# Optimization experiments

Hardware: AMD Instinct MI355X
Metric: run time of the kernel (lower is better)

## Reference

```python
import jax, jax.numpy as jnp
import numpy as np

HEADS = 12
EMBED = 768
HEAD_DIM = EMBED // HEADS


def setup_inputs() -> dict:
    key = jax.random.key(0)
    kx, kw, kb = jax.random.split(key, 3)
    x = jax.random.normal(kx, (8, 1024, EMBED), dtype=jnp.float32)
    # nn.Linear(embed, 3*embed): weight (3E, E), bias (3E,)
    W_qkv = jax.random.normal(kw, (3 * EMBED, EMBED), dtype=jnp.float32) * (1.0 / np.sqrt(EMBED))
    b_qkv = jax.random.normal(kb, (3 * EMBED,), dtype=jnp.float32) * 0.01
    return {"x": x, "W_qkv": W_qkv, "b_qkv": b_qkv}


def reference(x, W_qkv, b_qkv):
    b, n, e = x.shape
    qkv = x @ W_qkv.T + b_qkv                       # (b, n, 3E)
    qkv = qkv.reshape(b, n, HEADS, 3 * HEAD_DIM)    # (b, n, h, 3d)
    q, k, v = jnp.split(qkv, 3, axis=-1)            # each (b, n, h, d)
    scores = jnp.einsum('bihd,bjhd->bijh', q, k) / np.sqrt(HEAD_DIM)
    attn = jax.nn.softmax(scores, axis=-2)          # softmax over keys j (dim=-2)
    out = jnp.einsum('bijh,bjhd->bihd', attn, v)
    return out.reshape(b, n, e)
```

## Files before the change

kernel.cpp:

```cpp
#include <hip/hip_runtime.h>
#include <hip/hip_bf16.h>
#include <cstdint>

#define BATCH 8
#define SEQ   1024
#define EMB   768
#define HEADS 12
#define HDIM  64
#define C3    2304
#define MROWS (BATCH*SEQ)
#define KSLC  (EMB / 16)
#define XPACK_BLOCKS (MROWS * KSLC / 256)
#define WPACK_BLOCKS (C3 * KSLC / 256)

typedef __attribute__((ext_vector_type(8)))  short bf16x8;
typedef __attribute__((ext_vector_type(4)))  short bf16x4;
typedef __attribute__((ext_vector_type(4)))  float f32x4;
typedef __attribute__((ext_vector_type(16))) float f32x16;

static __device__ inline short f2bf(float f) {
    union { float f; uint32_t u; } v; v.f = f;
    uint32_t u = v.u + 0x7fff + ((v.u >> 16) & 1);
    return (short)(u >> 16);
}

__global__ __launch_bounds__(256) void pack_bf16(const float* __restrict__ x,
                                                 short* __restrict__ xb2,
                                                 const float* __restrict__ W,
                                                 short* __restrict__ Wb2) {
    const float* in;
    short* out;
    int tid;
    if (blockIdx.x < XPACK_BLOCKS) {
        in = x; out = xb2;
        tid = blockIdx.x * 256 + threadIdx.x;
    } else {
        in = W; out = Wb2;
        tid = (blockIdx.x - XPACK_BLOCKS) * 256 + threadIdx.x;
    }
    const int r    = tid & 31;
    const int ks   = (tid >> 5) % KSLC;
    const int tile = tid / (KSLC * 32);
    const int row  = tile * 32 + r;

    const float* src = in + (size_t)row * EMB + ks * 16;
    float4 v0 = ((const float4*)src)[0];
    float4 v1 = ((const float4*)src)[1];
    float4 v2 = ((const float4*)src)[2];
    float4 v3 = ((const float4*)src)[3];
    bf16x8 o0 = { f2bf(v0.x), f2bf(v0.y), f2bf(v0.z), f2bf(v0.w),
                  f2bf(v1.x), f2bf(v1.y), f2bf(v1.z), f2bf(v1.w) };
    bf16x8 o1 = { f2bf(v2.x), f2bf(v2.y), f2bf(v2.z), f2bf(v2.w),
                  f2bf(v3.x), f2bf(v3.y), f2bf(v3.z), f2bf(v3.w) };
    short* dst = out + (size_t)tid * 16;
    *(bf16x8*)(dst)     = o0;
    *(bf16x8*)(dst + 8) = o1;
}

__global__ __launch_bounds__(256) void qkv_gemm_mfma(const short* __restrict__ xb2,
                                                     const short* __restrict__ Wb2,
                                                     const float* __restrict__ bias,
                                                     short* __restrict__ qkvb) {
    const int g    = blockIdx.x;
    const int xcd  = g & 7;
    const int ring = g >> 3;
    const int by   = xcd * 8 + (ring & 7);
    const int bx   = ring >> 3;

    const int t = threadIdx.x;
    const int w = t >> 6;
    const int lane = t & 63;
    const int l5  = lane >> 5;
    const int r31 = lane & 31;
    const int m0 = by * 128, n0 = bx * 128;
    const int wm = (w & 1) * 64, wn = (w >> 1) * 64;

    const int laneoff = r31 * 16 + l5 * 8;
    const short* pa0 = xb2 + ((size_t)((m0 + wm) >> 5) * KSLC) * 512 + laneoff;
    const short* pa1 = pa0 + (size_t)KSLC * 512;
    const short* pb0 = Wb2 + ((size_t)((n0 + wn) >> 5) * KSLC) * 512 + laneoff;
    const short* pb1 = pb0 + (size_t)KSLC * 512;

    f32x16 acc[2][2] = {};

    #pragma unroll 4
    for (int ks = 0; ks < KSLC; ++ks) {
        bf16x8 a0 = *(const bf16x8*)(pa0 + ks * 512);
        bf16x8 a1 = *(const bf16x8*)(pa1 + ks * 512);
        bf16x8 b0 = *(const bf16x8*)(pb0 + ks * 512);
        bf16x8 b1 = *(const bf16x8*)(pb1 + ks * 512);
        acc[0][0] = __builtin_amdgcn_mfma_f32_32x32x16_bf16(a0, b0, acc[0][0], 0, 0, 0);
        acc[0][1] = __builtin_amdgcn_mfma_f32_32x32x16_bf16(a0, b1, acc[0][1], 0, 0, 0);
        acc[1][0] = __builtin_amdgcn_mfma_f32_32x32x16_bf16(a1, b0, acc[1][0], 0, 0, 0);
        acc[1][1] = __builtin_amdgcn_mfma_f32_32x32x16_bf16(a1, b1, acc[1][1], 0, 0, 0);
    }

    float bsv[2], scl[2];
    #pragma unroll
    for (int nt = 0; nt < 2; ++nt) {
        int n = n0 + wn + nt * 32 + r31;
        bsv[nt] = bias[n];
        scl[nt] = ((n % 192) < 64) ? 0.125f : 1.0f;
    }
    #pragma unroll
    for (int mt = 0; mt < 2; ++mt)
        #pragma unroll
        for (int nt = 0; nt < 2; ++nt) {
            int n = n0 + wn + nt * 32 + r31;
            #pragma unroll
            for (int reg = 0; reg < 16; ++reg) {
                int row = (reg & 3) + 8 * (reg >> 2) + 4 * l5;
                int m = m0 + wm + mt * 32 + row;
                float v = (acc[mt][nt][reg] + bsv[nt]) * scl[nt];
                qkvb[(size_t)m * C3 + n] = f2bf(v);
            }
        }
}

__global__ __launch_bounds__(256) void v_transpose(const short* __restrict__ qkvb,
                                                   short* __restrict__ vt) {
    __shared__ int Lt[64][65];

    const int bh = blockIdx.x;
    const int jt = blockIdx.y;
    const int b = bh / HEADS, h = bh % HEADS;
    const int t = threadIdx.x;
    const int j0 = jt * 64;
    const size_t base = (size_t)b * SEQ * C3 + (size_t)h * 192 + 128;

    #pragma unroll
    for (int p = 0; p < 2; ++p) {
        int idx = p * 256 + t;
        int j = idx >> 3, d0 = (idx & 7) * 8;
        bf16x8 v = *(const bf16x8*)(qkvb + base + (size_t)(j0 + j) * C3 + d0);
        #pragma unroll
        for (int u = 0; u < 8; ++u)
            Lt[d0 + u][j] = (int)(unsigned short)v[u];
    }
    __syncthreads();
    #pragma unroll
    for (int p = 0; p < 2; ++p) {
        int idx = p * 256 + t;
        int d = idx >> 3, c8 = (idx & 7) * 8;
        bf16x8 o;
        #pragma unroll
        for (int u = 0; u < 8; ++u)
            o[u] = (short)Lt[d][c8 + u];
        *(bf16x8*)(vt + ((size_t)bh * 64 + d) * SEQ + j0 + c8) = o;
    }
}

#define LDP 72

__global__ __launch_bounds__(256, 3) void attn_mfma(const short* __restrict__ qkvb,
                                                    const short* __restrict__ vt,
                                                    float* __restrict__ out) {
    __shared__ short Ks[64][LDP];
    __shared__ short Vt[64][LDP];
    __shared__ short Ps[128][LDP];

    const int g    = blockIdx.x;
    const int qt   = g / (BATCH * HEADS);
    const int bh   = g % (BATCH * HEADS);
    const int b    = bh / HEADS;
    const int h    = bh % HEADS;
    const int t    = threadIdx.x;
    const int w    = t >> 6;
    const int lane = t & 63;
    const int c    = lane & 15;
    const int q    = lane >> 4;
    const int i0   = qt * 128;

    const size_t base = (size_t)b * SEQ * C3 + (size_t)h * 192;
    const short* vtb = vt + (size_t)bh * 64 * SEQ;

    #pragma unroll
    for (int p = 0; p < 4; ++p) {
        int idx = p * 256 + t;
        int i = idx >> 3, d0 = (idx & 7) << 3;
        *(bf16x8*)&Ps[i][d0] =
            *(const bf16x8*)(qkvb + base + (size_t)(i0 + i) * C3 + d0);
    }
    __syncthreads();
    bf16x8 aq[2][2];
    #pragma unroll
    for (int s = 0; s < 2; ++s) {
        aq[s][0] = *(bf16x8*)&Ps[w * 32 + s * 16 + c][q * 8];
        aq[s][1] = *(bf16x8*)&Ps[w * 32 + s * 16 + c][32 + q * 8];
    }

    f32x4 o[2][4] = {};
    float l_acc[2] = {0.f, 0.f};

    for (int kt = 0; kt < 16; ++kt) {
        const int j0 = kt * 64;
        __syncthreads();
        #pragma unroll
        for (int p = 0; p < 2; ++p) {
            int idx = p * 256 + t;
            int j = idx >> 3, d0 = (idx & 7) << 3;
            *(bf16x8*)&Ks[j][d0] =
                *(const bf16x8*)(qkvb + base + 64 + (size_t)(j0 + j) * C3 + d0);
        }
        #pragma unroll
        for (int p = 0; p < 2; ++p) {
            int idx = p * 256 + t;
            int d = idx >> 3, j8 = (idx & 7) << 3;
            *(bf16x8*)&Vt[d][j8] =
                *(const bf16x8*)(vtb + (size_t)d * SEQ + j0 + j8);
        }
        __syncthreads();

        bf16x8 ka[4][2];
        #pragma unroll
        for (int mt = 0; mt < 4; ++mt) {
            ka[mt][0] = *(bf16x8*)&Ks[mt * 16 + c][q * 8];
            ka[mt][1] = *(bf16x8*)&Ks[mt * 16 + c][32 + q * 8];
        }

        f32x4 s[2][4];
        #pragma unroll
        for (int ss = 0; ss < 2; ++ss)
            #pragma unroll
            for (int mt = 0; mt < 4; ++mt) {
                f32x4 acc = {0.f, 0.f, 0.f, 0.f};
                acc = __builtin_amdgcn_mfma_f32_16x16x32_bf16(ka[mt][0], aq[ss][0], acc, 0, 0, 0);
                acc = __builtin_amdgcn_mfma_f32_16x16x32_bf16(ka[mt][1], aq[ss][1], acc, 0, 0, 0);
                s[ss][mt] = acc;
            }

        #pragma unroll
        for (int ss = 0; ss < 2; ++ss)
            #pragma unroll
            for (int mt = 0; mt < 4; ++mt) {
                float p0 = __expf(s[ss][mt][0]);
                float p1 = __expf(s[ss][mt][1]);
                float p2 = __expf(s[ss][mt][2]);
                float p3 = __expf(s[ss][mt][3]);
                l_acc[ss] += (p0 + p1) + (p2 + p3);
                bf16x4 pw = { f2bf(p0), f2bf(p1), f2bf(p2), f2bf(p3) };
                *(bf16x4*)&Ps[w * 32 + ss * 16 + c][mt * 16 + 4 * q] = pw;
            }

        bf16x8 vb[4][2];
        #pragma unroll
        for (int dt = 0; dt < 4; ++dt) {
            vb[dt][0] = *(bf16x8*)&Vt[dt * 16 + c][q * 8];
            vb[dt][1] = *(bf16x8*)&Vt[dt * 16 + c][32 + q * 8];
        }

        #pragma unroll
        for (int ss = 0; ss < 2; ++ss) {
            bf16x8 ap0 = *(bf16x8*)&Ps[w * 32 + ss * 16 + c][q * 8];
            bf16x8 ap1 = *(bf16x8*)&Ps[w * 32 + ss * 16 + c][32 + q * 8];
            #pragma unroll
            for (int dt = 0; dt < 4; ++dt) {
                o[ss][dt] = __builtin_amdgcn_mfma_f32_16x16x32_bf16(ap0, vb[dt][0], o[ss][dt], 0, 0, 0);
                o[ss][dt] = __builtin_amdgcn_mfma_f32_16x16x32_bf16(ap1, vb[dt][1], o[ss][dt], 0, 0, 0);
            }
        }
    }

    float linv[2][4];
    #pragma unroll
    for (int ss = 0; ss < 2; ++ss) {
        float v = l_acc[ss];
        v += __shfl_xor(v, 16, 64);
        v += __shfl_xor(v, 32, 64);
        #pragma unroll
        for (int r = 0; r < 4; ++r)
            linv[ss][r] = 1.0f / __shfl(v, 4 * q + r, 64);
    }

    #pragma unroll
    for (int ss = 0; ss < 2; ++ss)
        #pragma unroll
        for (int dt = 0; dt < 4; ++dt)
            #pragma unroll
            for (int r = 0; r < 4; ++r) {
                int i = w * 32 + ss * 16 + q * 4 + r;
                out[((size_t)b * SEQ + i0 + i) * EMB + h * HDIM + dt * 16 + c]
                    = o[ss][dt][r] * linv[ss][r];
            }
}

extern "C" void kernel_launch(void* const* d_in, const int* in_sizes, int n_in,
                              void* d_out, int out_size, void* d_ws, size_t ws_size,
                              hipStream_t stream) {
    const float* x    = (const float*)d_in[0];
    const float* W    = (const float*)d_in[1];
    const float* bias = (const float*)d_in[2];
    float* out = (float*)d_out;

    short* xb2  = (short*)d_ws;
    short* Wb2  = xb2 + (size_t)MROWS * EMB;
    short* qkvb = Wb2 + (size_t)C3 * EMB;
    short* vt   = qkvb + (size_t)MROWS * C3;

    pack_bf16<<<XPACK_BLOCKS + WPACK_BLOCKS, 256, 0, stream>>>(x, xb2, W, Wb2);

    qkv_gemm_mfma<<<1152, 256, 0, stream>>>(xb2, Wb2, bias, qkvb);

    dim3 g2(BATCH * HEADS, SEQ / 64);
    v_transpose<<<g2, 256, 0, stream>>>(qkvb, vt);

    attn_mfma<<<BATCH * HEADS * (SEQ / 128), 256, 0, stream>>>(qkvb, vt, out);
}
```

Measured before the change: 169.3 us.

## Stage QKV GEMM tiles through double-buffered LDS with direct global-to-LDS loads

The QKV projection GEMM previously streamed each wave's operand fragments straight from global memory, so a fragment shared by waves was fetched once per wave. It now double-buffers 128x32 A and B tiles in shared memory using global_load_lds, so loads overlap compute and the four waves reuse one copy. The pack kernel now emits a tile-contiguous, XOR-swizzled layout so the LDS reads avoid bank conflicts, and the MFMA shape moves from 32x32x16 to 16x16x32. The cost is LDS capacity, which may limit occupancy, and a barrier per k-step.

```diff
diff --git a/kernel.cpp b/kernel.cpp
--- a/kernel.cpp
+++ b/kernel.cpp
@@ -9,9 +9,11 @@
 #define HDIM  64
 #define C3    2304
 #define MROWS (BATCH*SEQ)
-#define KSLC  (EMB / 16)
-#define XPACK_BLOCKS (MROWS * KSLC / 256)
-#define WPACK_BLOCKS (C3 * KSLC / 256)
+#define NKT   (EMB / 32)
+#define MTILES (MROWS / 128)
+#define NTILES (C3 / 128)
+#define XPACK_BLOCKS (MTILES * NKT)
+#define WPACK_BLOCKS (NTILES * NKT)
 
 typedef __attribute__((ext_vector_type(8)))  short bf16x8;
 typedef __attribute__((ext_vector_type(4)))  short bf16x4;
@@ -22,6 +24,12 @@
     union { float f; uint32_t u; } v; v.f = f;
     uint32_t u = v.u + 0x7fff + ((v.u >> 16) & 1);
     return (short)(u >> 16);
+}
+
+static __device__ __forceinline__ void gload_lds16(const short* g, short* l) {
+    __builtin_amdgcn_global_load_lds(
+        (const __attribute__((address_space(1))) unsigned int*)g,
+        (__attribute__((address_space(3))) unsigned int*)l, 16, 0, 0);
 }
 
 __global__ __launch_bounds__(256) void pack_bf16(const float* __restrict__ x,
@@ -30,89 +38,121 @@
                                                  short* __restrict__ Wb2) {
     const float* in;
     short* out;
-    int tid;
+    int blk;
     if (blockIdx.x < XPACK_BLOCKS) {
-        in = x; out = xb2;
-        tid = blockIdx.x * 256 + threadIdx.x;
+        in = x; out = xb2; blk = blockIdx.x;
     } else {
-        in = W; out = Wb2;
-        tid = (blockIdx.x - XPACK_BLOCKS) * 256 + threadIdx.x;
-    }
-    const int r    = tid & 31;
-    const int ks   = (tid >> 5) % KSLC;
-    const int tile = tid / (KSLC * 32);
-    const int row  = tile * 32 + r;
-
-    const float* src = in + (size_t)row * EMB + ks * 16;
-    float4 v0 = ((const float4*)src)[0];
-    float4 v1 = ((const float4*)src)[1];
-    float4 v2 = ((const float4*)src)[2];
-    float4 v3 = ((const float4*)src)[3];
-    bf16x8 o0 = { f2bf(v0.x), f2bf(v0.y), f2bf(v0.z), f2bf(v0.w),
-                  f2bf(v1.x), f2bf(v1.y), f2bf(v1.z), f2bf(v1.w) };
-    bf16x8 o1 = { f2bf(v2.x), f2bf(v2.y), f2bf(v2.z), f2bf(v2.w),
-                  f2bf(v3.x), f2bf(v3.y), f2bf(v3.z), f2bf(v3.w) };
-    short* dst = out + (size_t)tid * 16;
-    *(bf16x8*)(dst)     = o0;
-    *(bf16x8*)(dst + 8) = o1;
-}
-
-__global__ __launch_bounds__(256) void qkv_gemm_mfma(const short* __restrict__ xb2,
-                                                     const short* __restrict__ Wb2,
+        in = W; out = Wb2; blk = blockIdx.x - XPACK_BLOCKS;
+    }
+    const int mt = blk / NKT;
+    const int kt = blk % NKT;
+    short* obase = out + (size_t)blk * 4096;
+
+    #pragma unroll
+    for (int p = 0; p < 2; ++p) {
+        int idx = p * 256 + threadIdx.x;
+        int r = idx >> 2, s = idx & 3;
+        const float* src = in + (size_t)(mt * 128 + r) * EMB + kt * 32 + s * 8;
+        float4 v0 = ((const float4*)src)[0];
+        float4 v1 = ((const float4*)src)[1];
+        bf16x8 o = { f2bf(v0.x), f2bf(v0.y), f2bf(v0.z), f2bf(v0.w),
+                     f2bf(v1.x), f2bf(v1.y), f2bf(v1.z), f2bf(v1.w) };
+        int S = ((4 * r + s) ^ (r & 7));
+        *(bf16x8*)(obase + S * 8) = o;
+    }
+}
+
+__global__ __launch_bounds__(256) void qkv_gemm_mfma(const short* __restrict__ Apk,
+                                                     const short* __restrict__ Bpk,
                                                      const float* __restrict__ bias,
                                                      short* __restrict__ qkvb) {
+    __shared__ short As[2][4096];
+    __shared__ short Bs[2][4096];
+
     const int g    = blockIdx.x;
     const int xcd  = g & 7;
     const int ring = g >> 3;
     const int by   = xcd * 8 + (ring & 7);
     const int bx   = ring >> 3;
 
-    const int t = threadIdx.x;
-    const int w = t >> 6;
+    const int t    = threadIdx.x;
+    const int w    = t >> 6;
     const int lane = t & 63;
-    const int l5  = lane >> 5;
-    const int r31 = lane & 31;
+    const int s4   = lane >> 4;
+    const int r15  = lane & 15;
     const int m0 = by * 128, n0 = bx * 128;
     const int wm = (w & 1) * 64, wn = (w >> 1) * 64;
 
-    const int laneoff = r31 * 16 + l5 * 8;
-    const short* pa0 = xb2 + ((size_t)((m0 + wm) >> 5) * KSLC) * 512 + laneoff;
-    const short* pa1 = pa0 + (size_t)KSLC * 512;
-    const short* pb0 = Wb2 + ((size_t)((n0 + wn) >> 5) * KSLC) * 512 + laneoff;
-    const short* pb1 = pb0 + (size_t)KSLC * 512;
-
-    f32x16 acc[2][2] = {};
-
-    #pragma unroll 4
-    for (int ks = 0; ks < KSLC; ++ks) {
-        bf16x8 a0 = *(const bf16x8*)(pa0 + ks * 512);
-        bf16x8 a1 = *(const bf16x8*)(pa1 + ks * 512);
-        bf16x8 b0 = *(const bf16x8*)(pb0 + ks * 512);
-        bf16x8 b1 = *(const bf16x8*)(pb1 + ks * 512);
-        acc[0][0] = __builtin_amdgcn_mfma_f32_32x32x16_bf16(a0, b0, acc[0][0], 0, 0, 0);
-        acc[0][1] = __builtin_amdgcn_mfma_f32_32x32x16_bf16(a0, b1, acc[0][1], 0, 0, 0);
-        acc[1][0] = __builtin_amdgcn_mfma_f32_32x32x16_bf16(a1, b0, acc[1][0], 0, 0, 0);
-        acc[1][1] = __builtin_amdgcn_mfma_f32_32x32x16_bf16(a1, b1, acc[1][1], 0, 0, 0);
-    }
-
-    float bsv[2], scl[2];
-    #pragma unroll
-    for (int nt = 0; nt < 2; ++nt) {
-        int n = n0 + wn + nt * 32 + r31;
-        bsv[nt] = bias[n];
-        scl[nt] = ((n % 192) < 64) ? 0.125f : 1.0f;
-    }
-    #pragma unroll
-    for (int mt = 0; mt < 2; ++mt)
-        #pragma unroll
-        for (int nt = 0; nt < 2; ++nt) {
-            int n = n0 + wn + nt * 32 + r31;
-            #pragma unroll
-            for (int reg = 0; reg < 16; ++reg) {
-                int row = (reg & 3) + 8 * (reg >> 2) + 4 * l5;
-                int m = m0 + wm + mt * 32 + row;
-                float v = (acc[mt][nt][reg] + bsv[nt]) * scl[nt];
-                qkvb[(size_t)m * C3 + n] = f2bf(v);
+    const short* Ab = Apk + (size_t)by * (NKT * 4096);
+    const short* Bb = Bpk + (size_t)bx * (NKT * 4096);
+
+    int offA[4], offB[4];
+    #pragma unroll
+    for (int i = 0; i < 4; ++i) {
+        int ra = wm + i * 16 + r15;
+        offA[i] = ((4 * ra + s4) ^ (ra & 7)) << 3;
+        int rb = wn + i * 16 + r15;
+        offB[i] = ((4 * rb + s4) ^ (rb & 7)) << 3;
+    }
+
+    const int seg0 = w * 2;
+
+#define STAGE(buf, kt) do {                                                   \
+        const short* _a = Ab + (size_t)(kt) * 4096;                           \
+        const short* _b = Bb + (size_t)(kt) * 4096;                           \
+        gload_lds16(_a + (seg0    ) * 512 + lane * 8, &As[buf][(seg0    ) * 512]); \
+        gload_lds16(_b + (seg0    ) * 512 + lane * 8, &Bs[buf][(seg0    ) * 512]); \
+        gload_lds16(_a + (seg0 + 1) * 512 + lane * 8, &As[buf][(seg0 + 1) * 512]); \
+        gload_lds16(_b + (seg0 + 1) * 512 + lane * 8, &Bs[buf][(seg0 + 1) * 512]); \
+    } while (0)
+
+    f32x4 acc[4][4] = {};
+
+#define COMPUTE(buf) do {                                                     \
+        bf16x8 af[4], bff[4];                                                 \
+        _Pragma("unroll")                                                     \
+        for (int i = 0; i < 4; ++i) {                                         \
+            af[i]  = *(const bf16x8*)&As[buf][offA[i]];                       \
+            bff[i] = *(const bf16x8*)&Bs[buf][offB[i]];                       \
+        }                                                                     \
+        _Pragma("unroll")                                                     \
+        for (int mi = 0; mi < 4; ++mi)                                        \
+            _Pragma("unroll")                                                 \
+            for (int ni = 0; ni < 4; ++ni)                                    \
+                acc[mi][ni] = __builtin_amdgcn_mfma_f32_16x16x32_bf16(        \
+                    af[mi], bff[ni], acc[mi][ni], 0, 0, 0);                   \
+    } while (0)
+
+    STAGE(0, 0);
+    __syncthreads();
+
+    for (int kt = 0; kt < NKT; kt += 2) {
+        STAGE(1, kt + 1);
+        COMPUTE(0);
+        __syncthreads();
+        if (kt + 2 < NKT) STAGE(0, kt + 2);
+        COMPUTE(1);
+        __syncthreads();
+    }
+#undef STAGE
+#undef COMPUTE
+
+    float bsv[4], scl[4];
+    #pragma unroll
+    for (int ni = 0; ni < 4; ++ni) {
+        int n = n0 + wn + ni * 16 + r15;
+        bsv[ni] = bias[n];
+        scl[ni] = ((n % 192) < 64) ? 0.125f : 1.0f;
+    }
+    #pragma unroll
+    for (int mi = 0; mi < 4; ++mi)
+        #pragma unroll
+        for (int ni = 0; ni < 4; ++ni) {
+            int n = n0 + wn + ni * 16 + r15;
+            #pragma unroll
+            for (int reg = 0; reg < 4; ++reg) {
+                int m = m0 + wm + mi * 16 + s4 * 4 + reg;
+                qkvb[(size_t)m * C3 + n] = f2bf((acc[mi][ni][reg] + bsv[ni]) * scl[ni]);
             }
         }
 }
```

After: 170.3 us. About the same (+0.6%).
